# Performance work log

Measured on AMD Instinct MI355X. Metric: run time of the kernel, lower is better.

The kernel has to match this reference:

```python
import jax, jax.numpy as jnp
import numpy as np

B, S, D, H = 4, 1024, 1024, 16
DH = D // H  # 64
SCALE = 1.0 / np.sqrt(DH)


def setup_inputs() -> dict:
    key = jax.random.key(0)
    ks = jax.random.split(key, 12)
    std = 0.02
    inp = {
        "query": jax.random.normal(ks[0], (B, S, D), jnp.float32),
        "key": jax.random.normal(ks[1], (B, S, D), jnp.float32),
        "value": jax.random.normal(ks[2], (B, S, D), jnp.float32),
        # all-ones mask: exercises masked_fill path without the NaN the
        # head-axis softmax would produce for any masked entry
        "mask": jnp.ones((1, S, S), jnp.int32),
        "Wq": jax.random.normal(ks[3], (D, D), jnp.float32) * std,
        "bq": jnp.zeros((D,), jnp.float32),
        "Wk": jax.random.normal(ks[4], (D, D), jnp.float32) * std,
        "bk": jnp.zeros((D,), jnp.float32),
        "Wv": jax.random.normal(ks[5], (D, D), jnp.float32) * std,
        "bv": jnp.zeros((D,), jnp.float32),
        "Wo": jax.random.normal(ks[6], (D, D), jnp.float32) * std,
        "bo": jnp.zeros((D,), jnp.float32),
    }
    return inp


def reference(query, key, value, mask, Wq, bq, Wk, bk, Wv, bv, Wo, bo):
    # project and split heads: [B, S, D] -> [B, S, H, DH]
    q = (query @ Wq + bq).reshape(B, S, H, DH)
    k = (key @ Wk + bk).reshape(B, S, H, DH)
    v = (value @ Wv + bv).reshape(B, S, H, DH)

    # scores [B, i, j, H]
    scores = jnp.einsum("bihd,bjhd->bijh", q, k) * SCALE
    # mask [1, i, j] broadcast over heads via trailing axis (unsqueeze(-1))
    scores = jnp.where(mask[..., None] == 0, -jnp.inf, scores)
    # faithful to source: nn.Softmax(dim=-1) on bijh layout -> softmax over HEADS
    attn = jax.nn.softmax(scores, axis=-1)
    # dropout in eval mode (identity)
    x = jnp.einsum("bijh,bjhd->bihd", attn, v).reshape(B, S, D)
    return x @ Wo + bo
```

## Files before the change

kernel.cpp:

```cpp
#include <hip/hip_runtime.h>
#include <hip/hip_bf16.h>


using f32x4  = __attribute__((ext_vector_type(4))) float;
using f32x2  = __attribute__((ext_vector_type(2))) float;
using bf16x8 = __attribute__((ext_vector_type(8))) short;
using bf16x4 = __attribute__((ext_vector_type(4))) short;

__device__ inline unsigned short f2b(float f){
    unsigned u = __float_as_uint(f);
    unsigned r = (u + 0x7fffu + ((u >> 16) & 1u)) >> 16;
    return (unsigned short)r;
}
__device__ inline float b2f(unsigned short s){
    return __uint_as_float(((unsigned)s) << 16);
}

#define GLL16(gp, lp) __builtin_amdgcn_global_load_lds( \
    (const __attribute__((address_space(1))) void*)(gp), \
    (__attribute__((address_space(3))) void*)(lp), 16, 0, 0)

#define LGKM0 do { asm volatile("s_waitcnt lgkmcnt(0)" ::: "memory"); \
                   __builtin_amdgcn_sched_barrier(0); } while(0)
#define BAR   do { __builtin_amdgcn_s_barrier(); \
                   __builtin_amdgcn_sched_barrier(0); } while(0)

__global__ __launch_bounds__(256) void convert_qkv(
    const float* __restrict__ q, const float* __restrict__ k, const float* __restrict__ v,
    unsigned short* __restrict__ dst)
{
    const long gid = (long)blockIdx.x * 256 + threadIdx.x;
    const int  t   = (int)(gid >> 20);
    const long off = (gid & 1048575) << 2;
    const float* src = (t == 0) ? q : (t == 1) ? k : v;
    const float4 x = *(const float4*)(src + off);
    ushort4 o;
    o.x = f2b(x.x); o.y = f2b(x.y); o.z = f2b(x.z); o.w = f2b(x.w);
    *(ushort4*)(dst + (long)t * 4194304 + off) = o;
}

__global__ __launch_bounds__(256) void wtrans(
    const float* __restrict__ w0, const float* __restrict__ w1,
    const float* __restrict__ w2, const float* __restrict__ w3,
    unsigned short* __restrict__ out)
{
    const float* W = (blockIdx.z == 0) ? w0 : (blockIdx.z == 1) ? w1 : (blockIdx.z == 2) ? w2 : w3;
    unsigned short* O = out + (long)blockIdx.z * 1048576;
    __shared__ float t[32][33];
    const int n0 = blockIdx.x * 32, k0 = blockIdx.y * 32;
    const int tx = threadIdx.x, ty = threadIdx.y;
    #pragma unroll
    for (int i = 0; i < 4; i++)
        t[ty + 8*i][tx] = W[(long)(k0 + ty + 8*i) * 1024 + n0 + tx];
    __syncthreads();
    #pragma unroll
    for (int i = 0; i < 4; i++)
        O[(long)(n0 + ty + 8*i) * 1024 + k0 + tx] = f2b(t[tx][ty + 8*i]);
}

template<int OUTF32>
__device__ __forceinline__ void gemm_body(
    const unsigned short* __restrict__ A,
    const unsigned short* __restrict__ BT,
    const float* __restrict__ bias,
    void* __restrict__ Cout, int N, int K,
    unsigned short* As, unsigned short* Bs)
{
    const int tid  = threadIdx.x;
    const int wave = tid >> 6, lane = tid & 63;
    const int l15  = lane & 15, l4 = lane >> 4;
    const int wr   = wave >> 1, wc = wave & 1;
    const long rowBase = (long)blockIdx.x * 128;
    const long colBase = (long)blockIdx.y * 128;

    f32x4 acc[4][4];
    #pragma unroll
    for (int m = 0; m < 4; m++)
        #pragma unroll
        for (int n = 0; n < 4; n++)
            acc[m][n] = (f32x4){0.f, 0.f, 0.f, 0.f};

    const int c0    = wave * 2;
    const int srow0 = c0 * 16 + (lane >> 2);
    const int srow1 = srow0 + 16;
    const int skk   = (lane & 3) * 8;

    for (int k0 = 0; k0 < K; k0 += 32) {
        GLL16(A  + (rowBase + srow0) * K + k0 + skk, As + c0 * 512);
        GLL16(A  + (rowBase + srow1) * K + k0 + skk, As + (c0 + 1) * 512);
        GLL16(BT + (colBase + srow0) * K + k0 + skk, Bs + c0 * 512);
        GLL16(BT + (colBase + srow1) * K + k0 + skk, Bs + (c0 + 1) * 512);
        __syncthreads();
        bf16x8 af[4], bfr[4];
        #pragma unroll
        for (int m = 0; m < 4; m++)
            af[m] = *(const bf16x8*)(As + (wr*64 + m*16 + l15) * 32 + l4 * 8);
        #pragma unroll
        for (int n = 0; n < 4; n++)
            bfr[n] = *(const bf16x8*)(Bs + (wc*64 + n*16 + l15) * 32 + l4 * 8);
        #pragma unroll
        for (int m = 0; m < 4; m++)
            #pragma unroll
            for (int n = 0; n < 4; n++)
                acc[m][n] = __builtin_amdgcn_mfma_f32_16x16x32_bf16(af[m], bfr[n], acc[m][n], 0, 0, 0);
        __syncthreads();
    }

    #pragma unroll
    for (int m = 0; m < 4; m++) {
        const long row = rowBase + wr*64 + m*16 + l4*4;
        #pragma unroll
        for (int n = 0; n < 4; n++) {
            const long col = colBase + wc*64 + n*16 + l15;
            const float bv = bias[col];
            #pragma unroll
            for (int r = 0; r < 4; r++) {
                const float vv = acc[m][n][r] + bv;
                if (OUTF32) ((float*)Cout)[(row + r) * N + col] = vv;
                else        ((unsigned short*)Cout)[(row + r) * N + col] = f2b(vv);
            }
        }
    }
}

__global__ __launch_bounds__(256) void gemm_bias_f32(
    const unsigned short* __restrict__ A,
    const unsigned short* __restrict__ BT,
    const float* __restrict__ bias,
    float* __restrict__ Cout, int N, int K)
{
    __shared__ unsigned short As[128 * 32];
    __shared__ unsigned short Bs[128 * 32];
    gemm_body<1>(A, BT, bias, (void*)Cout, N, K, As, Bs);
}

__global__ __launch_bounds__(256) void gemm3(
    const unsigned short* __restrict__ Abase,
    const unsigned short* __restrict__ WT,
    const float* __restrict__ bq, const float* __restrict__ bk, const float* __restrict__ bv,
    unsigned short* __restrict__ Cpk)
{
    __shared__ unsigned short As[128 * 32];
    __shared__ unsigned short Bs[128 * 32];
    const int z = blockIdx.z;
    const unsigned short* A  = Abase + (long)z * 4194304;
    const unsigned short* BT = WT    + (long)z * 1048576;
    unsigned short*       C  = Cpk   + (long)z * 4194304;
    const float* bias = (z == 0) ? bq : (z == 1) ? bk : bv;

    const int tid  = threadIdx.x;
    const int wave = tid >> 6, lane = tid & 63;
    const int l15  = lane & 15, l4 = lane >> 4;
    const int wr   = wave >> 1, wc = wave & 1;
    const int rowBase = blockIdx.x * 128;
    const int colBase = blockIdx.y * 128;
    const int K = 1024;

    f32x4 acc[4][4];
    #pragma unroll
    for (int m = 0; m < 4; m++)
        #pragma unroll
        for (int n = 0; n < 4; n++)
            acc[m][n] = (f32x4){0.f, 0.f, 0.f, 0.f};

    const int c0    = wave * 2;
    const int srow0 = c0 * 16 + (lane >> 2);
    const int srow1 = srow0 + 16;
    const int skk   = (lane & 3) * 8;

    for (int k0 = 0; k0 < K; k0 += 32) {
        GLL16(A  + (long)(rowBase + srow0) * K + k0 + skk, As + c0 * 512);
        GLL16(A  + (long)(rowBase + srow1) * K + k0 + skk, As + (c0 + 1) * 512);
        GLL16(BT + (long)(colBase + srow0) * K + k0 + skk, Bs + c0 * 512);
        GLL16(BT + (long)(colBase + srow1) * K + k0 + skk, Bs + (c0 + 1) * 512);
        __syncthreads();
        bf16x8 af[4], bfr[4];
        #pragma unroll
        for (int m = 0; m < 4; m++)
            af[m] = *(const bf16x8*)(As + (wr*64 + m*16 + l15) * 32 + l4 * 8);
        #pragma unroll
        for (int n = 0; n < 4; n++)
            bfr[n] = *(const bf16x8*)(Bs + (wc*64 + n*16 + l15) * 32 + l4 * 8);
        #pragma unroll
        for (int m = 0; m < 4; m++)
            #pragma unroll
            for (int n = 0; n < 4; n++)
                acc[m][n] = __builtin_amdgcn_mfma_f32_16x16x32_bf16(af[m], bfr[n], acc[m][n], 0, 0, 0);
        __syncthreads();
    }

    #pragma unroll
    for (int m = 0; m < 4; m++) {
        const int R0 = rowBase + wr*64 + m*16 + l4*4;
        #pragma unroll
        for (int n = 0; n < 4; n++) {
            const int c = colBase + wc*64 + n*16 + l15;
            const float bv2 = bias[c];
            #pragma unroll
            for (int r = 0; r < 4; r++) {
                const int R = R0 + r;
                const float vv = acc[m][n][r] + bv2;
                long addr;
                if (z == 2)
                    addr = (long)(R >> 5) * 32768 + (c >> 4) * 512
                         + (((R >> 3) & 3) * 16 + (c & 15)) * 8 + (R & 7);
                else
                    addr = (long)(R >> 4) * 16384 + (c >> 5) * 512
                         + (((c >> 3) & 3) * 16 + (R & 15)) * 8 + (c & 7);
                C[addr] = f2b(vv);
            }
        }
    }
}

__global__ __launch_bounds__(512, 2) void attn_fused(
    const unsigned short* __restrict__ Qf_,
    const unsigned short* __restrict__ Kf_,
    const unsigned short* __restrict__ Vf_,
    const int* __restrict__ mask,
    unsigned short* __restrict__ P0,
    unsigned short* __restrict__ P1)
{
    __shared__ __align__(16) unsigned char smem[73728];
    float*         Se = (float*)smem;
    float*         So = (float*)(smem + 36864);
    unsigned char* Pb = smem;

    const int tid = threadIdx.x, w = tid >> 6, lane = tid & 63;
    const int l15 = lane & 15, l4 = lane >> 4;
    const int h0  = 2 * w;
    const int sxor = h0 ^ (l4 << 2);

    const int bid = blockIdx.x;
    const int wg  = (bid & 7) * 32 + (bid >> 3);
    const int b   = wg >> 6;
    const int jh  = (wg >> 5) & 1;
    const int i0  = (wg & 31) << 5;

    const unsigned short* Kfb = Kf_ + (long)b * 1048576;
    const unsigned short* Vfb = Vf_ + (long)b * 1048576;
    unsigned short* Pout = (jh == 0) ? P0 : P1;

    const int si = tid >> 4, sj = tid & 15;
    const int xorv = si & 12;
    const int mrow = (i0 + si) * 1024 + (jh << 9);

    bf16x8 qf[2][2][2];
    #pragma unroll
    for (int is = 0; is < 2; is++)
        #pragma unroll
        for (int hh = 0; hh < 2; hh++)
            #pragma unroll
            for (int ks = 0; ks < 2; ks++)
                qf[is][hh][ks] = *(const bf16x8*)(Qf_ + (long)(b*64 + (i0 >> 4) + is) * 16384
                                                  + ((h0 + hh) * 2 + ks) * 512 + lane * 8);

#define LOAD_KF(JT) do { \
    _Pragma("unroll") \
    for (int t_ = 0; t_ < 2; t_++) \
        _Pragma("unroll") \
        for (int hh = 0; hh < 2; hh++) \
            _Pragma("unroll") \
            for (int ks = 0; ks < 2; ks++) \
                kf[t_][hh][ks] = *(const bf16x8*)(Kfb + ((JT) + t_) * 16384 \
                                                   + ((h0 + hh) * 2 + ks) * 512 + lane * 8); \
    } while(0)

#define LOAD_VF(JG) do { \
    _Pragma("unroll") \
    for (int hh = 0; hh < 2; hh++) \
        _Pragma("unroll") \
        for (int n = 0; n < 4; n++) \
            vf[hh][n] = *(const bf16x8*)(Vfb + (long)(JG) * 32768 \
                                           + ((h0 + hh) * 4 + n) * 512 + lane * 8); \
    } while(0)

    bf16x8 kf[2][2][2];
    bf16x8 vf[2][4];
    LOAD_KF(jh*32);
    LOAD_VF(jh*16);

    f32x4 acc[2][2][4];
    #pragma unroll
    for (int is = 0; is < 2; is++)
        #pragma unroll
        for (int hh = 0; hh < 2; hh++)
            #pragma unroll
            for (int n = 0; n < 4; n++)
                acc[is][hh][n] = (f32x4){0.f, 0.f, 0.f, 0.f};

    for (int g = 0; g < 16; ++g) {
        const int mke = mask[mrow + g * 32 + sj];
        const int mko = mask[mrow + g * 32 + 16 + sj];

        __builtin_amdgcn_s_setprio(1);
        #pragma unroll
        for (int t_ = 0; t_ < 2; t_++) {
            float* St = t_ ? So : Se;
            #pragma unroll
            for (int is = 0; is < 2; is++) {
                f32x4 sv0 = (f32x4){0.f,0.f,0.f,0.f}, sv1 = (f32x4){0.f,0.f,0.f,0.f};
                sv0 = __builtin_amdgcn_mfma_f32_16x16x32_bf16(qf[is][0][0], kf[t_][0][0], sv0, 0, 0, 0);
                sv0 = __builtin_amdgcn_mfma_f32_16x16x32_bf16(qf[is][0][1], kf[t_][0][1], sv0, 0, 0, 0);
                sv1 = __builtin_amdgcn_mfma_f32_16x16x32_bf16(qf[is][1][0], kf[t_][1][0], sv1, 0, 0, 0);
                sv1 = __builtin_amdgcn_mfma_f32_16x16x32_bf16(qf[is][1][1], kf[t_][1][1], sv1, 0, 0, 0);
                #pragma unroll
                for (int r = 0; r < 4; r++) {
                    const int ij = (is*16 + l4*4 + r) * 16 + l15;
                    f32x2 pr; pr[0] = sv0[r]; pr[1] = sv1[r];
                    *(f32x2*)(St + ij * 18 + sxor) = pr;
                }
            }
        }
        __builtin_amdgcn_s_setprio(0);
        LGKM0; BAR;

        if (g < 15) LOAD_KF(jh*32 + (g + 1) * 2);

        unsigned pe[8];
        {
            const float* sp = Se + tid * 18;
            float tv[16];
            #pragma unroll
            for (int q_ = 0; q_ < 8; q_++) {
                const f32x2 t2 = *(const f32x2*)(sp + q_ * 2);
                tv[q_*2] = t2[0]; tv[q_*2+1] = t2[1];
            }
            float Z = 0.f;
            #pragma unroll
            for (int h = 0; h < 16; h++) {
                float x = tv[h] * 0.18033688f;
                if (mke == 0) x = -__builtin_inff();
                float e; asm("v_exp_f32 %0, %1" : "=v"(e) : "v"(x));
                tv[h] = e; Z += e;
            }
            float inv; asm("v_rcp_f32 %0, %1" : "=v"(inv) : "v"(Z));
            #pragma unroll
            for (int h = 0; h < 8; h++) {
                const unsigned lo = (__float_as_uint(tv[2*h]   * inv) + 0x8000u) >> 16;
                const unsigned hi = (__float_as_uint(tv[2*h+1] * inv) + 0x8000u) >> 16;
                pe[h] = lo | (hi << 16);
            }
        }
        BAR;
        #pragma unroll
        for (int h = 0; h < 16; h++) {
            const unsigned short pv = (unsigned short)((h & 1) ? (pe[h >> 1] >> 16) : pe[h >> 1]);
            *(unsigned short*)(Pb + (h ^ xorv) * 2304 + si * 72 + sj * 2) = pv;
        }

        {
            const float* sp = So + tid * 18;
            float tv[16];
            #pragma unroll
            for (int q_ = 0; q_ < 8; q_++) {
                const f32x2 t2 = *(const f32x2*)(sp + q_ * 2);
                tv[q_*2] = t2[0]; tv[q_*2+1] = t2[1];
            }
            float Z = 0.f;
            #pragma unroll
            for (int h = 0; h < 16; h++) {
                float x = tv[h] * 0.18033688f;
                if (mko == 0) x = -__builtin_inff();
                float e; asm("v_exp_f32 %0, %1" : "=v"(e) : "v"(x));
                tv[h] = e; Z += e;
            }
            float inv; asm("v_rcp_f32 %0, %1" : "=v"(inv) : "v"(Z));
            #pragma unroll
            for (int h = 0; h < 16; h++) {
                const unsigned p16 = (__float_as_uint(tv[h] * inv) + 0x8000u) >> 16;
                *(unsigned short*)(Pb + (h ^ xorv) * 2304 + si * 72 + 32 + sj * 2) = (unsigned short)p16;
            }
        }
        LGKM0; BAR;

        {
            bf16x8 pa[2][2];
            #pragma unroll
            for (int is = 0; is < 2; is++)
                #pragma unroll
                for (int hh = 0; hh < 2; hh++) {
                    const unsigned char* pr = Pb + (h0 + hh) * 2304 + (is*16 + l15) * 72 + l4 * 16;
                    bf16x4 lo = *(const bf16x4*)(pr);
                    bf16x4 hi = *(const bf16x4*)(pr + 8);
                    pa[is][hh] = (bf16x8){lo[0],lo[1],lo[2],lo[3], hi[0],hi[1],hi[2],hi[3]};
                }
            __builtin_amdgcn_s_setprio(1);
            #pragma unroll
            for (int is = 0; is < 2; is++)
                #pragma unroll
                for (int hh = 0; hh < 2; hh++)
                    #pragma unroll
                    for (int n = 0; n < 4; n++)
                        acc[is][hh][n] = __builtin_amdgcn_mfma_f32_16x16x32_bf16(pa[is][hh], vf[hh][n], acc[is][hh][n], 0, 0, 0);
            __builtin_amdgcn_s_setprio(0);
        }
        if (g < 15) {
            LOAD_VF(jh*16 + g + 1);
            BAR;
        }
    }

    #pragma unroll
    for (int is = 0; is < 2; is++)
        #pragma unroll
        for (int hh = 0; hh < 2; hh++)
            #pragma unroll
            for (int n = 0; n < 4; n++)
                #pragma unroll
                for (int r = 0; r < 4; r++) {
                    const long row = b * 1024 + i0 + is * 16 + l4 * 4 + r;
                    Pout[row * 1024 + (h0 + hh) * 64 + n * 16 + l15] = f2b(acc[is][hh][n][r]);
                }
#undef LOAD_KF
#undef LOAD_VF
}

__global__ __launch_bounds__(256) void addp(
    unsigned short* __restrict__ P0, const unsigned short* __restrict__ P1)
{
    const long i = ((long)blockIdx.x * 256 + threadIdx.x) * 8;
    ushort4 a0 = *(const ushort4*)(P0 + i);
    ushort4 a1 = *(const ushort4*)(P0 + i + 4);
    ushort4 b0 = *(const ushort4*)(P1 + i);
    ushort4 b1 = *(const ushort4*)(P1 + i + 4);
    ushort4 o0, o1;
    o0.x = f2b(b2f(a0.x) + b2f(b0.x)); o0.y = f2b(b2f(a0.y) + b2f(b0.y));
    o0.z = f2b(b2f(a0.z) + b2f(b0.z)); o0.w = f2b(b2f(a0.w) + b2f(b0.w));
    o1.x = f2b(b2f(a1.x) + b2f(b1.x)); o1.y = f2b(b2f(a1.y) + b2f(b1.y));
    o1.z = f2b(b2f(a1.z) + b2f(b1.z)); o1.w = f2b(b2f(a1.w) + b2f(b1.w));
    *(ushort4*)(P0 + i) = o0;
    *(ushort4*)(P0 + i + 4) = o1;
}

extern "C" void kernel_launch(void* const* d_in, const int* in_sizes, int n_in,
                              void* d_out, int out_size, void* d_ws, size_t ws_size,
                              hipStream_t stream)
{
    const float* q    = (const float*)d_in[0];
    const float* k    = (const float*)d_in[1];
    const float* v    = (const float*)d_in[2];
    const int*   mask = (const int*)  d_in[3];
    const float* Wq   = (const float*)d_in[4];
    const float* bq   = (const float*)d_in[5];
    const float* Wk   = (const float*)d_in[6];
    const float* bk   = (const float*)d_in[7];
    const float* Wv   = (const float*)d_in[8];
    const float* bv   = (const float*)d_in[9];
    const float* Wo   = (const float*)d_in[10];
    const float* bo   = (const float*)d_in[11];

    unsigned short* ws = (unsigned short*)d_ws;
    const long MS = 1048576;
    unsigned short* WT  = ws;
    unsigned short* Xq  = ws + 4*MS;
    unsigned short* Xk  = ws + 8*MS;
    unsigned short* Xv  = ws + 12*MS;
    unsigned short* Qf  = ws + 16*MS;
    unsigned short* Kf  = ws + 20*MS;
    unsigned short* Vf  = ws + 24*MS;
    unsigned short* P0  = Xk;
    unsigned short* P1  = Xq;

    convert_qkv<<<12288, 256, 0, stream>>>(q, k, v, Xq);
    wtrans<<<dim3(32, 32, 4), dim3(32, 8), 0, stream>>>(Wq, Wk, Wv, Wo, WT);
    gemm3<<<dim3(32, 8, 3), 256, 0, stream>>>(Xq, WT, bq, bk, bv, Qf);
    attn_fused<<<256, 512, 0, stream>>>(Qf, Kf, Vf, mask, P0, P1);
    addp<<<2048, 256, 0, stream>>>(P0, P1);
    gemm_bias_f32<<<dim3(32, 8), 256, 0, stream>>>(P0, WT + 3*MS, bo, (float*)d_out, 1024, 1024);
}
```

Before: 151.0 us.

## Double GEMM K-tile to 64 and XOR-swizzle LDS layout

Both the QKV projection GEMM and the output GEMM now stage 64-wide K tiles per iteration instead of 32, which halves the number of barrier pairs and loop iterations. The shared-memory layout uses an XOR swizzle on the 16-byte chunk index, applied both when staging with global_load_lds and when reading fragments, to avoid LDS bank conflicts. LDS use per block doubles to 32 KB, which may limit occupancy, and more fragment registers are held live per iteration.

```diff
diff --git a/kernel.cpp b/kernel.cpp
--- a/kernel.cpp
+++ b/kernel.cpp
@@ -80,29 +80,34 @@
         for (int n = 0; n < 4; n++)
             acc[m][n] = (f32x4){0.f, 0.f, 0.f, 0.f};
 
-    const int c0    = wave * 2;
-    const int srow0 = c0 * 16 + (lane >> 2);
-    const int srow1 = srow0 + 16;
-    const int skk   = (lane & 3) * 8;
-
-    for (int k0 = 0; k0 < K; k0 += 32) {
-        GLL16(A  + (rowBase + srow0) * K + k0 + skk, As + c0 * 512);
-        GLL16(A  + (rowBase + srow1) * K + k0 + skk, As + (c0 + 1) * 512);
-        GLL16(BT + (colBase + srow0) * K + k0 + skk, Bs + c0 * 512);
-        GLL16(BT + (colBase + srow1) * K + k0 + skk, Bs + (c0 + 1) * 512);
+    const int srow = wave * 32 + (lane >> 3);
+    const int skk  = (((lane & 7) ^ ((lane >> 3) & 7))) * 8;
+    const int fx   = (l15 & 7);
+
+    for (int k0 = 0; k0 < K; k0 += 64) {
+        #pragma unroll
+        for (int u = 0; u < 4; u++) {
+            GLL16(A  + (rowBase + srow + u*8) * K + k0 + skk, As + (wave*32 + u*8) * 64);
+            GLL16(BT + (colBase + srow + u*8) * K + k0 + skk, Bs + (wave*32 + u*8) * 64);
+        }
         __syncthreads();
-        bf16x8 af[4], bfr[4];
+        bf16x8 af[4][2], bfr[4][2];
         #pragma unroll
         for (int m = 0; m < 4; m++)
-            af[m] = *(const bf16x8*)(As + (wr*64 + m*16 + l15) * 32 + l4 * 8);
-        #pragma unroll
-        for (int n = 0; n < 4; n++)
-            bfr[n] = *(const bf16x8*)(Bs + (wc*64 + n*16 + l15) * 32 + l4 * 8);
-        #pragma unroll
-        for (int m = 0; m < 4; m++)
-            #pragma unroll
-            for (int n = 0; n < 4; n++)
-                acc[m][n] = __builtin_amdgcn_mfma_f32_16x16x32_bf16(af[m], bfr[n], acc[m][n], 0, 0, 0);
+            #pragma unroll
+            for (int kk = 0; kk < 2; kk++) {
+                af[m][kk]  = *(const bf16x8*)(As + (wr*64 + m*16 + l15) * 64
+                                               + (((kk*4 + l4) ^ fx) * 8));
+                bfr[m][kk] = *(const bf16x8*)(Bs + (wc*64 + m*16 + l15) * 64
+                                               + (((kk*4 + l4) ^ fx) * 8));
+            }
+        #pragma unroll
+        for (int kk = 0; kk < 2; kk++)
+            #pragma unroll
+            for (int m = 0; m < 4; m++)
+                #pragma unroll
+                for (int n = 0; n < 4; n++)
+                    acc[m][n] = __builtin_amdgcn_mfma_f32_16x16x32_bf16(af[m][kk], bfr[n][kk], acc[m][n], 0, 0, 0);
         __syncthreads();
     }
 
@@ -129,8 +134,8 @@
     const float* __restrict__ bias,
     float* __restrict__ Cout, int N, int K)
 {
-    __shared__ unsigned short As[128 * 32];
-    __shared__ unsigned short Bs[128 * 32];
+    __shared__ unsigned short As[128 * 64];
+    __shared__ unsigned short Bs[128 * 64];
     gemm_body<1>(A, BT, bias, (void*)Cout, N, K, As, Bs);
 }
 
@@ -140,8 +145,8 @@
     const float* __restrict__ bq, const float* __restrict__ bk, const float* __restrict__ bv,
     unsigned short* __restrict__ Cpk)
 {
-    __shared__ unsigned short As[128 * 32];
-    __shared__ unsigned short Bs[128 * 32];
+    __shared__ unsigned short As[128 * 64];
+    __shared__ unsigned short Bs[128 * 64];
     const int z = blockIdx.z;
     const unsigned short* A  = Abase + (long)z * 4194304;
     const unsigned short* BT = WT    + (long)z * 1048576;
@@ -163,29 +168,34 @@
         for (int n = 0; n < 4; n++)
             acc[m][n] = (f32x4){0.f, 0.f, 0.f, 0.f};
 
-    const int c0    = wave * 2;
-    const int srow0 = c0 * 16 + (lane >> 2);
-    const int srow1 = srow0 + 16;
-    const int skk   = (lane & 3) * 8;
-
-    for (int k0 = 0; k0 < K; k0 += 32) {
-        GLL16(A  + (long)(rowBase + srow0) * K + k0 + skk, As + c0 * 512);
-        GLL16(A  + (long)(rowBase + srow1) * K + k0 + skk, As + (c0 + 1) * 512);
-        GLL16(BT + (long)(colBase + srow0) * K + k0 + skk, Bs + c0 * 512);
-        GLL16(BT + (long)(colBase + srow1) * K + k0 + skk, Bs + (c0 + 1) * 512);
+    const int srow = wave * 32 + (lane >> 3);
+    const int skk  = (((lane & 7) ^ ((lane >> 3) & 7))) * 8;
+    const int fx   = (l15 & 7);
+
+    for (int k0 = 0; k0 < K; k0 += 64) {
+        #pragma unroll
+        for (int u = 0; u < 4; u++) {
+            GLL16(A  + (long)(rowBase + srow + u*8) * K + k0 + skk, As + (wave*32 + u*8) * 64);
+            GLL16(BT + (long)(colBase + srow + u*8) * K + k0 + skk, Bs + (wave*32 + u*8) * 64);
+        }
         __syncthreads();
-        bf16x8 af[4], bfr[4];
+        bf16x8 af[4][2], bfr[4][2];
         #pragma unroll
         for (int m = 0; m < 4; m++)
-            af[m] = *(const bf16x8*)(As + (wr*64 + m*16 + l15) * 32 + l4 * 8);
-        #pragma unroll
-        for (int n = 0; n < 4; n++)
-            bfr[n] = *(const bf16x8*)(Bs + (wc*64 + n*16 + l15) * 32 + l4 * 8);
-        #pragma unroll
-        for (int m = 0; m < 4; m++)
-            #pragma unroll
-            for (int n = 0; n < 4; n++)
-                acc[m][n] = __builtin_amdgcn_mfma_f32_16x16x32_bf16(af[m], bfr[n], acc[m][n], 0, 0, 0);
+            #pragma unroll
+            for (int kk = 0; kk < 2; kk++) {
+                af[m][kk]  = *(const bf16x8*)(As + (wr*64 + m*16 + l15) * 64
+                                               + (((kk*4 + l4) ^ fx) * 8));
+                bfr[m][kk] = *(const bf16x8*)(Bs + (wc*64 + m*16 + l15) * 64
+                                               + (((kk*4 + l4) ^ fx) * 8));
+            }
+        #pragma unroll
+        for (int kk = 0; kk < 2; kk++)
+            #pragma unroll
+            for (int m = 0; m < 4; m++)
+                #pragma unroll
+                for (int n = 0; n < 4; n++)
+                    acc[m][n] = __builtin_amdgcn_mfma_f32_16x16x32_bf16(af[m][kk], bfr[n][kk], acc[m][n], 0, 0, 0);
         __syncthreads();
     }
 
```

Result: faster. 144.5 us (-4.3%).
